# Kernel tuning notes

Hardware: AMD Instinct MI355X
Metric: run time of the kernel (lower is better)

Reference implementation:

```python
import jax, jax.numpy as jnp
import numpy as np

B, L, C, H, W = 2, 16, 16, 64, 64


def setup_inputs() -> dict:
    key = jax.random.key(0)
    k1, k2 = jax.random.split(key)
    # flows scaled so cumulative normalized-coordinate flows mostly stay in [-1, 1]
    flows = jax.random.normal(k1, (B, L, 2, H, W), dtype=jnp.float32) * 0.05
    images = jax.random.normal(k2, (B, L, C, H, W), dtype=jnp.float32)
    return {"flows": flows, "images": images}


def _bilinear_sample(images, gx, gy):
    # images: [B, Lj, C, H, W]; gx, gy: [B, Li, Lj, H, W] normalized coords in [-1, 1]
    # Replicates torch.nn.functional.grid_sample(mode='bilinear',
    # padding_mode='zeros', align_corners=False).
    Bs, Lj, Cs, Hs, Ws = images.shape
    ix = ((gx + 1.0) * Ws - 1.0) * 0.5  # pixel x coord
    iy = ((gy + 1.0) * Hs - 1.0) * 0.5  # pixel y coord
    x0f = jnp.floor(ix)
    y0f = jnp.floor(iy)
    wx = ix - x0f  # weight toward x0+1 (differentiable w.r.t. flow)
    wy = iy - y0f
    x0 = x0f.astype(jnp.int32)
    y0 = y0f.astype(jnp.int32)
    img_flat = images.reshape(Bs, Lj, Cs, Hs * Ws)

    def gather(xi, yi):
        valid = (xi >= 0) & (xi < Ws) & (yi >= 0) & (yi < Hs)  # [B,Li,Lj,H,W]
        lin = jnp.clip(yi, 0, Hs - 1) * Ws + jnp.clip(xi, 0, Ws - 1)
        lin_t = jnp.transpose(lin, (0, 2, 1, 3, 4))  # [B,Lj,Li,H,W]
        # per (b, j): gather [C, HW] at indices [Li, H, W] -> [C, Li, H, W]
        v = jax.vmap(jax.vmap(lambda im, l: im[:, l]))(img_flat, lin_t)
        v = jnp.transpose(v, (0, 3, 1, 2, 4, 5))  # [B,Li,Lj,C,H,W]
        return v * valid[:, :, :, None, :, :].astype(v.dtype)

    v00 = gather(x0, y0)
    v01 = gather(x0 + 1, y0)
    v10 = gather(x0, y0 + 1)
    v11 = gather(x0 + 1, y0 + 1)
    wX = wx[:, :, :, None, :, :]
    wY = wy[:, :, :, None, :, :]
    return (v00 * (1.0 - wX) * (1.0 - wY) + v01 * wX * (1.0 - wY)
            + v10 * (1.0 - wX) * wY + v11 * wX * wY)


def reference(flows, images):
    Bs, Ls, _, Hs, Ws = flows.shape
    dt = flows.dtype
    cum = jnp.cumsum(flows, axis=1)  # [B,L,2,H,W]
    # rel[b, i, j] = cum[b, i] - cum[b, j]  -> [B,Li,Lj,2,H,W]
    rel = cum[:, :, None] - cum[:, None, :]
    # base sampling grid (pixel centers in normalized coords)
    gx_base = (jnp.arange(Ws, dtype=dt) + 0.5) * (2.0 / Ws) - 1.0  # [W]
    gy_base = (jnp.arange(Hs, dtype=dt) + 0.5) * (2.0 / Hs) - 1.0  # [H]
    gx = gx_base + rel[:, :, :, 0]              # [B,Li,Lj,H,W]
    gy = gy_base[:, None] + rel[:, :, :, 1]     # [B,Li,Lj,H,W]
    gx = jnp.remainder(gx + 1.0, 2.0) - 1.0     # wrap x into [-1, 1)
    warped = _bilinear_sample(images, gx, gy)   # [B,Li,Lj,C,H,W]
    mask = jnp.tril(jnp.ones((Ls, Ls), dtype=dt))
    # causal accumulate over source index j
    return jnp.einsum('bijchw,ij->bichw', warped, mask)
```

## Files before the change

kernel.cpp:

```cpp
#include <hip/hip_runtime.h>
#include <hip/hip_fp16.h>

#define BB 2
#define LL 16
#define CC 16
#define HH 64
#define WW 64
#define HWSZ (HH * WW)

__device__ __forceinline__ float2 cvt2(unsigned int u) {
    __half2 h = *reinterpret_cast<const __half2*>(&u);
    return __half22float2(h);
}

__global__ __launch_bounds__(256) void gsp_prep(
    const float* __restrict__ images,
    const float* __restrict__ flows,
    uint4* __restrict__ h16,
    float4* __restrict__ cum4)
{
    if (blockIdx.x < 1024) {
        const int gid  = blockIdx.x * 256 + threadIdx.x;
        const int half = gid & 1;
        const int pix  = (gid >> 1) & (HWSZ - 1);
        const int bl   = gid >> 13;

        const float* src = images + (size_t)(bl * CC + half * 8) * HWSZ + pix;
        unsigned short hs[8];
        #pragma unroll
        for (int m = 0; m < 8; ++m) {
            __half h = __float2half(src[(size_t)m * HWSZ]);
            hs[m] = *reinterpret_cast<unsigned short*>(&h);
        }
        uint4 v;
        v.x = (unsigned)hs[0] | ((unsigned)hs[1] << 16);
        v.y = (unsigned)hs[2] | ((unsigned)hs[3] << 16);
        v.z = (unsigned)hs[4] | ((unsigned)hs[5] << 16);
        v.w = (unsigned)hs[6] | ((unsigned)hs[7] << 16);
        h16[((size_t)bl * HWSZ + pix) * 2 + half] = v;
        return;
    }

    const int u  = (blockIdx.x - 1024) * 256 + threadIdx.x;
    const int b  = u >> 12;
    const int px = u & (HWSZ - 1);
    const float* fb = flows + (size_t)b * LL * 2 * HWSZ + px;
    float cx = 0.0f, cy = 0.0f;
    float4 o[8];
    #pragma unroll
    for (int l = 0; l < LL; ++l) {
        cx += fb[(size_t)l * 2 * HWSZ];
        cy += fb[(size_t)l * 2 * HWSZ + HWSZ];
        if (l & 1) { o[l >> 1].z = cx; o[l >> 1].w = cy; }
        else       { o[l >> 1].x = cx; o[l >> 1].y = cy; }
    }
    float4* ob = cum4 + ((size_t)b * HWSZ + px) * 8;
    #pragma unroll
    for (int k2 = 0; k2 < 8; ++k2) ob[k2] = o[k2];
}

__device__ __forceinline__ void jstep(
    float cjx, float cjy, float cix, float ciy,
    float gxb, float gyb, int xc, int half,
    const uint4* __restrict__ jb,
    uint4& v0, uint4& v1, float& w0, float& w1)
{
    float gx = gxb + (cix - cjx);
    float gy = gyb + (ciy - cjy);
    float tt = gx + 1.0f;
    tt = tt - floorf(tt * 0.5f) * 2.0f;
    gx = tt - 1.0f;

    const float ix = ((gx + 1.0f) * WW - 1.0f) * 0.5f;
    const float iy = ((gy + 1.0f) * HH - 1.0f) * 0.5f;
    const float x0f = floorf(ix);
    const float y0f = floorf(iy);
    const float fx = ix - x0f;
    const float fy = iy - y0f;
    const int x0 = (int)x0f;
    const int y0 = (int)y0f;

    const int  xr = x0 + xc;
    const bool vx = (xr >= 0) && (xr < WW);
    const int  cx = min(max(xr, 0), WW - 1);
    const float wx = (xc ? fx : (1.0f - fx)) * (vx ? 1.0f : 0.0f);

    const int y1i = y0 + 1;
    const bool vy0 = (y0 >= 0) && (y0 < HH);
    const bool vy1 = (y1i >= 0) && (y1i < HH);
    const int cy0 = min(max(y0, 0), HH - 1);
    const int cy1 = min(max(y1i, 0), HH - 1);

    v0 = jb[(cy0 * WW + cx) * 2 + half];
    v1 = jb[(cy1 * WW + cx) * 2 + half];
    w0 = wx * (1.0f - fy) * (vy0 ? 1.0f : 0.0f);
    w1 = wx * fy * (vy1 ? 1.0f : 0.0f);
}

__device__ __forceinline__ void accum(const uint4 v, const float wv, float acc[8]) {
    const float2 p0 = cvt2(v.x), p1 = cvt2(v.y);
    const float2 p2 = cvt2(v.z), p3 = cvt2(v.w);
    acc[0] += wv * p0.x;  acc[1] += wv * p0.y;
    acc[2] += wv * p1.x;  acc[3] += wv * p1.y;
    acc[4] += wv * p2.x;  acc[5] += wv * p2.y;
    acc[6] += wv * p3.x;  acc[7] += wv * p3.y;
}

__global__ __launch_bounds__(256, 5) void gsp_main(
    const uint4*  __restrict__ h16,
    const float4* __restrict__ cum4,
    float* __restrict__ out)
{
    __shared__ float2 scum[64][16];

    const int idx  = blockIdx.x;
    const int xcd  = idx & 7;
    const int k    = idx >> 3;
    const int i    = 15 - (k >> 4);
    const int b    = (k >> 3) & 1;
    const int tile = xcd * 8 + (k & 7);

    const int sub  = threadIdx.x & 3;
    const int half = sub & 1;
    const int xc   = sub >> 1;
    const int pl   = threadIdx.x >> 2;
    const int px   = tile * 64 + pl;
    const int h = px >> 6;
    const int w = px & (WW - 1);

    {
        const float4* cb = cum4 + ((size_t)b * HWSZ + tile * 64) * 8;
        #pragma unroll
        for (int t = 0; t < 2; ++t) {
            const int g  = threadIdx.x * 2 + t;
            const float4 v = cb[g];
            const int pp = g >> 3;
            const int ll = (g & 7) * 2;
            scum[pp][(ll + pp) & 15]     = make_float2(v.x, v.y);
            scum[pp][(ll + 1 + pp) & 15] = make_float2(v.z, v.w);
        }
    }
    __syncthreads();

    const float2 ci = scum[pl][(i + pl) & 15];
    const float cix = ci.x, ciy = ci.y;

    const float gxb = (w + 0.5f) * (2.0f / WW) - 1.0f;
    const float gyb = (h + 0.5f) * (2.0f / HH) - 1.0f;

    const uint4* h16_b = h16 + (size_t)(b * LL) * HWSZ * 2;

    float acc[8];
    #pragma unroll
    for (int m = 0; m < 8; ++m) acc[m] = 0.0f;

    if (i > 0) {
        uint4 v0c, v1c; float w0c, w1c;
        {
            const float2 cj = scum[pl][(0 + pl) & 15];
            jstep(cj.x, cj.y, cix, ciy, gxb, gyb, xc, half,
                  h16_b, v0c, v1c, w0c, w1c);
        }
        for (int j = 1; j < i; ++j) {
            const float2 cj = scum[pl][(j + pl) & 15];
            uint4 v0n, v1n; float w0n, w1n;
            jstep(cj.x, cj.y, cix, ciy, gxb, gyb, xc, half,
                  h16_b + (size_t)j * HWSZ * 2, v0n, v1n, w0n, w1n);
            accum(v0c, w0c, acc);
            accum(v1c, w1c, acc);
            v0c = v0n; v1c = v1n; w0c = w0n; w1c = w1n;
        }
        accum(v0c, w0c, acc);
        accum(v1c, w1c, acc);
    }

    #pragma unroll
    for (int m = 0; m < 8; ++m) acc[m] += __shfl_xor(acc[m], 2, 64);

    float s0 = xc ? acc[4] : acc[0];
    float s1 = xc ? acc[5] : acc[1];
    float s2 = xc ? acc[6] : acc[2];
    float s3 = xc ? acc[7] : acc[3];

    {
        const uint2* h2 = (const uint2*)h16;
        const uint2 idv = h2[(((size_t)(b * LL + i) * HWSZ + px) * 2 + half) * 2 + xc];
        const float2 p0 = cvt2(idv.x), p1 = cvt2(idv.y);
        s0 += p0.x; s1 += p0.y; s2 += p1.x; s3 += p1.y;
    }

    const int q = half * 2 + xc;
    float* op = out + ((size_t)(b * LL + i) * CC + q * 4) * HWSZ + px;
    __builtin_nontemporal_store(s0, op + 0 * HWSZ);
    __builtin_nontemporal_store(s1, op + 1 * HWSZ);
    __builtin_nontemporal_store(s2, op + 2 * HWSZ);
    __builtin_nontemporal_store(s3, op + 3 * HWSZ);
}

extern "C" void kernel_launch(void* const* d_in, const int* in_sizes, int n_in,
                              void* d_out, int out_size, void* d_ws, size_t ws_size,
                              hipStream_t stream) {
    const float* flows  = (const float*)d_in[0];
    const float* images = (const float*)d_in[1];
    float* out = (float*)d_out;
    uint4*  h16  = (uint4*)d_ws;
    float4* cum4 = (float4*)((char*)d_ws + (size_t)4 * 1024 * 1024);

    gsp_prep<<<1056, 256, 0, stream>>>(images, flows, h16, cum4);

    gsp_main<<<2048, 256, 0, stream>>>(h16, cum4, out);
}
```

Measured before the change: 76.64 us.

## Deepen gather prefetch to two stages and hoist identity-term load

Turns the software pipeline over source frames j from one stage of prefetch into two, so gathers for j+1 and j+2 are in flight while frame j is accumulated. The identity (diagonal) load is issued before the barrier so its latency overlaps the shared-memory setup. It also drops the min-blocks-per-CU occupancy hint from the launch bounds, letting the compiler use more registers for the extra in-flight loads, which may lower occupancy.

```diff
diff --git a/kernel.cpp b/kernel.cpp
--- a/kernel.cpp
+++ b/kernel.cpp
@@ -106,7 +106,7 @@
     acc[6] += wv * p3.x;  acc[7] += wv * p3.y;
 }
 
-__global__ __launch_bounds__(256, 5) void gsp_main(
+__global__ __launch_bounds__(256) void gsp_main(
     const uint4*  __restrict__ h16,
     const float4* __restrict__ cum4,
     float* __restrict__ out)
@@ -140,6 +140,10 @@
             scum[pp][(ll + 1 + pp) & 15] = make_float2(v.z, v.w);
         }
     }
+
+    const uint2* h2 = (const uint2*)h16;
+    const uint2 idv = h2[(((size_t)(b * LL + i) * HWSZ + px) * 2 + half) * 2 + xc];
+
     __syncthreads();
 
     const float2 ci = scum[pl][(i + pl) & 15];
@@ -155,23 +159,35 @@
     for (int m = 0; m < 8; ++m) acc[m] = 0.0f;
 
     if (i > 0) {
-        uint4 v0c, v1c; float w0c, w1c;
+        uint4 a0, a1, b0, b1;
+        float wa0 = 0.0f, wa1 = 0.0f, wb0 = 0.0f, wb1 = 0.0f;
+        b0 = b1 = make_uint4(0u, 0u, 0u, 0u);
+
         {
             const float2 cj = scum[pl][(0 + pl) & 15];
             jstep(cj.x, cj.y, cix, ciy, gxb, gyb, xc, half,
-                  h16_b, v0c, v1c, w0c, w1c);
-        }
-        for (int j = 1; j < i; ++j) {
+                  h16_b, a0, a1, wa0, wa1);
+        }
+        if (i > 1) {
+            const float2 cj = scum[pl][(1 + pl) & 15];
+            jstep(cj.x, cj.y, cix, ciy, gxb, gyb, xc, half,
+                  h16_b + (size_t)HWSZ * 2, b0, b1, wb0, wb1);
+        }
+        #pragma unroll 2
+        for (int j = 2; j < i; ++j) {
+            accum(a0, wa0, acc);
+            accum(a1, wa1, acc);
+            a0 = b0; a1 = b1; wa0 = wb0; wa1 = wb1;
             const float2 cj = scum[pl][(j + pl) & 15];
-            uint4 v0n, v1n; float w0n, w1n;
             jstep(cj.x, cj.y, cix, ciy, gxb, gyb, xc, half,
-                  h16_b + (size_t)j * HWSZ * 2, v0n, v1n, w0n, w1n);
-            accum(v0c, w0c, acc);
-            accum(v1c, w1c, acc);
-            v0c = v0n; v1c = v1n; w0c = w0n; w1c = w1n;
-        }
-        accum(v0c, w0c, acc);
-        accum(v1c, w1c, acc);
+                  h16_b + (size_t)j * HWSZ * 2, b0, b1, wb0, wb1);
+        }
+        accum(a0, wa0, acc);
+        accum(a1, wa1, acc);
+        if (i > 1) {
+            accum(b0, wb0, acc);
+            accum(b1, wb1, acc);
+        }
     }
 
     #pragma unroll
@@ -183,8 +199,6 @@
     float s3 = xc ? acc[7] : acc[3];
 
     {
-        const uint2* h2 = (const uint2*)h16;
-        const uint2 idv = h2[(((size_t)(b * LL + i) * HWSZ + px) * 2 + half) * 2 + xc];
         const float2 p0 = cvt2(idv.x), p1 = cvt2(idv.y);
         s0 += p0.x; s1 += p0.y; s2 += p1.x; s3 += p1.y;
     }
```

Result: no change. 76.72 us (+0.1%).
